# Kernel tuning notes

Hardware: AMD Instinct MI355X
Metric: run time of the kernel (lower is better)

The kernel has to match this reference:

```python
import jax, jax.numpy as jnp
import numpy as np

B, S, D_IN = 2, 2048, 1024
H = 16
HD = 64  # head_dim = d_out // head_cnt


def setup_inputs() -> dict:
    key = jax.random.key(0)
    kx, kq, kk, kv = jax.random.split(key, 4)
    x = jax.random.normal(kx, (B, S, D_IN), dtype=jnp.float32)
    # Per-head Q/K/V projection weights, stacked: [H, d_in, head_dim].
    # Matches nn.Linear(d_in, head_out) per head (qkv_bias=False), scaled like
    # a typical init.
    sc = 1.0 / np.sqrt(D_IN)
    Wq = jax.random.normal(kq, (H, D_IN, HD), dtype=jnp.float32) * sc
    Wk = jax.random.normal(kk, (H, D_IN, HD), dtype=jnp.float32) * sc
    Wv = jax.random.normal(kv, (H, D_IN, HD), dtype=jnp.float32) * sc
    return {"x": x, "Wq": Wq, "Wk": Wk, "Wv": Wv}


def reference(x, Wq, Wk, Wv):
    # Batched multi-head causal attention equivalent to the per-head loop +
    # torch.cat(dim=-1): head h's output occupies slice [h*HD:(h+1)*HD].
    q = jnp.einsum("bsd,hde->bhse", x, Wq)  # [B,H,S,HD]
    k = jnp.einsum("bsd,hde->bhse", x, Wk)
    v = jnp.einsum("bsd,hde->bhse", x, Wv)
    scale = 1.0 / jnp.sqrt(jnp.asarray(HD, dtype=x.dtype))
    scores = jnp.einsum("bhse,bhte->bhst", q, k) * scale  # [B,H,S,S]
    seq = x.shape[1]
    causal = jnp.tril(jnp.ones((seq, seq), dtype=bool))
    scores = jnp.where(causal, scores, jnp.asarray(-jnp.inf, dtype=scores.dtype))
    attn = jax.nn.softmax(scores, axis=-1)  # dropout = 0.0 -> identity
    ctx = jnp.einsum("bhst,bhte->bhse", attn, v)  # [B,H,S,HD]
    # concat heads on last dim
    b, h, s, e = ctx.shape
    return ctx.transpose(0, 2, 1, 3).reshape(b, s, h * e)
```

## Files before the change

kernel.cpp:

```cpp
#include <hip/hip_runtime.h>


#define DI   1024
#define HD   64
#define NH   16
#define SEQ  2048
#define NB   2

typedef unsigned short u16;
typedef unsigned short us8 __attribute__((ext_vector_type(8)));
typedef unsigned short us4 __attribute__((ext_vector_type(4)));
typedef unsigned int   u32x2 __attribute__((ext_vector_type(2)));
typedef short bf8 __attribute__((ext_vector_type(8)));
typedef float f4 __attribute__((ext_vector_type(4)));

#define MFMA16(a, b, c) __builtin_amdgcn_mfma_f32_16x16x32_bf16((a), (b), (c), 0, 0, 0)

#if __has_builtin(__builtin_amdgcn_exp2f)
#define EXP2(x) __builtin_amdgcn_exp2f(x)
#else
#define EXP2(x) exp2f(x)
#endif

#if __has_builtin(__builtin_amdgcn_perm)
#define PKHI(a, b) __builtin_amdgcn_perm((a), (b), 0x07060302u)
#else
__device__ __forceinline__ unsigned PKHI(unsigned a, unsigned b) {
  return (b >> 16) | (a & 0xffff0000u);
}
#endif

__device__ __forceinline__ u16 f2bf(float f) {
  unsigned u = __float_as_uint(f);
  u += 0x7fffu + ((u >> 16) & 1u);
  return (u16)(u >> 16);
}

__device__ __forceinline__ void async16(const u16* g, u16* l) {
  __builtin_amdgcn_global_load_lds((const __attribute__((address_space(1))) void*)g,
                                   (__attribute__((address_space(3))) void*)l,
                                   16, 0, 0);
}

__global__ __launch_bounds__(256) void prep_k(const float* __restrict__ x,
                                              const float* __restrict__ Wq,
                                              const float* __restrict__ Wk,
                                              const float* __restrict__ Wv,
                                              u16* __restrict__ xb,
                                              u16* __restrict__ Wt) {
  __shared__ __align__(16) u16 tile[64][72];
  const int bid = blockIdx.x;
  if (bid < 2048) {
    const int i = (bid * 256 + threadIdx.x) * 8;
    float4 v0 = *(const float4*)(x + i);
    float4 v1 = *(const float4*)(x + i + 4);
    us8 o;
    o[0] = f2bf(v0.x); o[1] = f2bf(v0.y); o[2] = f2bf(v0.z); o[3] = f2bf(v0.w);
    o[4] = f2bf(v1.x); o[5] = f2bf(v1.y); o[6] = f2bf(v1.z); o[7] = f2bf(v1.w);
    *(us8*)(xb + i) = o;
    return;
  }
  const int idx = bid - 2048;
  const int mh = idx >> 4;
  const int d0 = (idx & 15) * 64;
  const int mat = mh >> 4, h = mh & 15;
  const float* W = (mat == 0 ? Wq : (mat == 1 ? Wk : Wv)) + (size_t)h * DI * HD;
  const int t = threadIdx.x;
  {
    const int r = t >> 2, c = (t & 3) * 16;
    const float* src = W + (size_t)(d0 + r) * HD + c;
    #pragma unroll
    for (int j = 0; j < 4; j++) {
      float4 v = *(const float4*)(src + j * 4);
      tile[r][c + j * 4 + 0] = f2bf(v.x);
      tile[r][c + j * 4 + 1] = f2bf(v.y);
      tile[r][c + j * 4 + 2] = f2bf(v.z);
      tile[r][c + j * 4 + 3] = f2bf(v.w);
    }
  }
  __syncthreads();
  {
    const int e = t >> 2, c = (t & 3) * 16;
    __align__(16) u16 tmp[16];
    #pragma unroll
    for (int i = 0; i < 16; i++) tmp[i] = tile[c + i][e];
    u16* dst = Wt + ((size_t)mh * HD + e) * DI + d0 + c;
    *(us8*)dst       = *(us8*)&tmp[0];
    *(us8*)(dst + 8) = *(us8*)&tmp[8];
  }
}

__global__ __launch_bounds__(256) void proj_k(const u16* __restrict__ x,
                                              const u16* __restrict__ Wt,
                                              u16* __restrict__ Qo,
                                              u16* __restrict__ Ko,
                                              u16* __restrict__ Vo) {
  __shared__ __align__(16) u16 xs[128 * 64];
  __shared__ __align__(16) u16 ws[128 * 64];
  const int m0 = blockIdx.x * 128, n0 = blockIdx.y * 128;
  const int tid = threadIdx.x, w = tid >> 6, lane = tid & 63;
  const int l15 = lane & 15, quad = lane >> 4;
  const int lrow = lane >> 3, lch = lane & 7;
  const int l7 = l15 & 7;

  f4 acc[4][4];
  #pragma unroll
  for (int i = 0; i < 4; i++)
    #pragma unroll
    for (int j = 0; j < 4; j++) {
      f4 z = {0.f, 0.f, 0.f, 0.f};
      acc[i][j] = z;
    }

  const u16* xg = x  + (size_t)(m0 + lrow) * DI + ((lch ^ lrow) * 8);
  const u16* wg = Wt + (size_t)(n0 + lrow) * DI + ((lch ^ lrow) * 8);

  for (int k0 = 0; k0 < DI; k0 += 64) {
    #pragma unroll
    for (int i = 0; i < 4; i++) {
      const int r0 = i * 32 + w * 8;
      async16(xg + (size_t)r0 * DI + k0, &xs[r0 * 64]);
      async16(wg + (size_t)r0 * DI + k0, &ws[r0 * 64]);
    }
    __syncthreads();
    #pragma unroll
    for (int ks = 0; ks < 64; ks += 32) {
      const int c0 = (ks >> 3) + quad;
      bf8 af[4], bfr[4];
      #pragma unroll
      for (int i = 0; i < 4; i++)
        af[i] = *(const bf8*)&xs[((w >> 1) * 64 + i * 16 + l15) * 64 + ((c0 ^ l7) * 8)];
      #pragma unroll
      for (int i = 0; i < 4; i++)
        bfr[i] = *(const bf8*)&ws[((w & 1) * 64 + i * 16 + l15) * 64 + ((c0 ^ l7) * 8)];
      #pragma unroll
      for (int mi = 0; mi < 4; mi++)
        #pragma unroll
        for (int ni = 0; ni < 4; ni++)
          acc[mi][ni] = MFMA16(af[mi], bfr[ni], acc[mi][ni]);
    }
    __syncthreads();
  }

  const int mat = n0 >> 10;
  const int nf0 = n0 + (w & 1) * 64;
  const float qscale = 0.125f * 1.44269504088896340736f;
  #pragma unroll
  for (int mi = 0; mi < 4; mi++) {
    const int mrow = m0 + (w >> 1) * 64 + mi * 16 + quad * 4;
    const int b = mrow >> 11, sb = mrow & (SEQ - 1);
    #pragma unroll
    for (int ni = 0; ni < 4; ni++) {
      const int nf = nf0 + ni * 16;
      const int h = (nf >> 6) & 15;
      const int e = (nf & 63) + l15;
      if (mat == 2) {
        __align__(8) u16 pk[4];
        #pragma unroll
        for (int r = 0; r < 4; r++) pk[r] = f2bf(acc[mi][ni][r]);
        *(us4*)(Vo + (((size_t)b * NH + h) * HD + e) * SEQ + sb) = *(us4*)pk;
      } else {
        u16* O = mat ? Ko : Qo;
        const float sc = mat ? 1.0f : qscale;
        #pragma unroll
        for (int r = 0; r < 4; r++)
          O[(((size_t)b * NH + h) * SEQ + sb + r) * HD + e] = f2bf(acc[mi][ni][r] * sc);
      }
    }
  }
}

__global__ __launch_bounds__(256, 2) void attn_k(const u16* __restrict__ Qo,
                                                 const u16* __restrict__ Ko,
                                                 const u16* __restrict__ Vo,
                                                 float* __restrict__ out) {
  __shared__ __align__(16) u16 Ks[2 * 128 * 64];
  __shared__ __align__(16) u16 Vs[2 * 64 * 128];
  __shared__ __align__(16) u16 Ps[4 * 16 * 128];
  const int ia = blockIdx.x;
  const int ib = 31 - ia;
  const int bh = blockIdx.y;
  const int b = bh >> 4, h = bh & 15;
  const int tid = threadIdx.x, w = tid >> 6, lane = tid & 63;
  const int l15 = lane & 15, quad = lane >> 4;
  const int qh = quad >> 1, ql = quad & 1;

  const u16* Qb = Qo + (size_t)bh * SEQ * HD;
  const u16* Kb = Ko + (size_t)bh * SEQ * HD;
  const u16* Vb = Vo + (size_t)bh * HD * SEQ;

  const int qrowA = ia * 64 + w * 16 + l15;
  const int qrowB = ib * 64 + w * 16 + l15;
  bf8 bqA0 = *(const bf8*)(Qb + (size_t)qrowA * HD + quad * 8);
  bf8 bqA1 = *(const bf8*)(Qb + (size_t)qrowA * HD + 32 + quad * 8);
  bf8 bqB0 = *(const bf8*)(Qb + (size_t)qrowB * HD + quad * 8);
  bf8 bqB1 = *(const bf8*)(Qb + (size_t)qrowB * HD + 32 + quad * 8);

  f4 oA[4], oB[4], lA, lB;
  #pragma unroll
  for (int i = 0; i < 4; i++) {
    f4 z = {0.f, 0.f, 0.f, 0.f};
    oA[i] = z; oB[i] = z;
  }
  {
    f4 z = {0.f, 0.f, 0.f, 0.f};
    lA = z; lB = z;
  }
  const bf8 ones = {0x3F80, 0x3F80, 0x3F80, 0x3F80, 0x3F80, 0x3F80, 0x3F80, 0x3F80};

  const int nA = ia / 2 + 1, nB = ib / 2 + 1;

  const u16* ksp0 = &Ks[l15 * 64 + ((quad ^ (l15 & 7)) * 8)];
  const u16* ksp1 = &Ks[l15 * 64 + (((quad + 4) ^ (l15 & 7)) * 8)];
  const u16* vsp[4];
  #pragma unroll
  for (int tc = 0; tc < 4; tc++)
    vsp[tc] = &Vs[l15 * 128 + (((tc * 4 + quad) ^ l15) * 8)];
  u16* const psw = &Ps[w * 2048 + l15 * 128 + ql * 4];
  const u16* prp[4];
  #pragma unroll
  for (int tc = 0; tc < 4; tc++)
    prp[tc] = &Ps[w * 2048 + l15 * 128 + (((tc * 4 + quad) ^ l15) * 8)];

  const int kl = lane >> 3, kc = lane & 7;
  const int vl = lane >> 4, vc = lane & 15;
  const u16* kg = Kb + (size_t)(w * 32 + kl) * HD + ((kc ^ kl) * 8);
  const u16* vg[4];
  u16* ldsK[4];
  u16* ldsV[4];
  #pragma unroll
  for (int i = 0; i < 4; i++) {
    const int vr = w * 16 + i * 4;
    const int f = (i * 4 + vl) & 15;
    vg[i] = Vb + (size_t)(vr + vl) * SEQ + ((vc ^ f) * 8);
    ldsK[i] = &Ks[(w * 32 + i * 8) * 64];
    ldsV[i] = &Vs[vr * 128];
  }

  const int mqA = qrowA - (nA - 1) * 128 - quad * 4;
  const int mqB = qrowB - (nB - 1) * 128 - quad * 4;

  auto pphase = [&](f4* s, bool domask, int mq) {
    #pragma unroll
    for (int mf = 0; mf < 8; mf++) {
      f4 sv = s[mf];
      if (domask) {
        #pragma unroll
        for (int r = 0; r < 4; r++)
          sv[r] = (mf * 16 + r <= mq) ? sv[r] : -1e30f;
      }
      const unsigned p0 = __float_as_uint(EXP2(sv[0]));
      const unsigned p1 = __float_as_uint(EXP2(sv[1]));
      const unsigned p2 = __float_as_uint(EXP2(sv[2]));
      const unsigned p3 = __float_as_uint(EXP2(sv[3]));
      u32x2 pk = {PKHI(p1, p0), PKHI(p3, p2)};
      *(u32x2*)(psw + ((((mf << 1) | qh) ^ l15) * 8)) = pk;
    }
  };

  #pragma unroll
  for (int i = 0; i < 4; i++) {
    async16(kg + i * 512, ldsK[i]);
    async16(vg[i], ldsV[i]);
  }
  kg += 128 * HD;
  #pragma unroll
  for (int i = 0; i < 4; i++) vg[i] += 128;

  for (int it = 0; it < nB; it++) {
    const int cb = (it & 1) * 8192;
    __syncthreads();
    if (it + 1 < nB) {
      const int nb = 8192 - cb;
      #pragma unroll
      for (int i = 0; i < 4; i++) {
        async16(kg + i * 512, ldsK[i] + nb);
        async16(vg[i], ldsV[i] + nb);
      }
      kg += 128 * HD;
      #pragma unroll
      for (int i = 0; i < 4; i++) vg[i] += 128;
    }
    const bool doA = (it < nA);

    f4 sA[8], sB[8];
    #pragma unroll
    for (int mf = 0; mf < 8; mf++) {
      bf8 ak0 = *(const bf8*)(ksp0 + cb + mf * 1024);
      bf8 ak1 = *(const bf8*)(ksp1 + cb + mf * 1024);
      f4 z = {0.f, 0.f, 0.f, 0.f};
      f4 tb = MFMA16(ak0, bqB0, z);
      sB[mf] = MFMA16(ak1, bqB1, tb);
      if (doA) {
        f4 ta = MFMA16(ak0, bqA0, z);
        sA[mf] = MFMA16(ak1, bqA1, ta);
      }
    }

    pphase(sB, it == nB - 1, mqB);
    #pragma unroll
    for (int tc = 0; tc < 4; tc++) {
      bf8 pf = *(const bf8*)(prp[tc]);
      lB = MFMA16(ones, pf, lB);
      #pragma unroll
      for (int ef = 0; ef < 4; ef++) {
        bf8 vf = *(const bf8*)(vsp[tc] + cb + ef * 2048);
        oB[ef] = MFMA16(vf, pf, oB[ef]);
      }
    }
    if (doA) {
      pphase(sA, it == nA - 1, mqA);
      #pragma unroll
      for (int tc = 0; tc < 4; tc++) {
        bf8 pf = *(const bf8*)(prp[tc]);
        lA = MFMA16(ones, pf, lA);
        #pragma unroll
        for (int ef = 0; ef < 4; ef++) {
          bf8 vf = *(const bf8*)(vsp[tc] + cb + ef * 2048);
          oA[ef] = MFMA16(vf, pf, oA[ef]);
        }
      }
    }
  }

  const float invA = 1.0f / lA[0];
  const float invB = 1.0f / lB[0];
  float* opA = out + ((size_t)b * SEQ + qrowA) * (NH * HD) + h * HD + quad * 4;
  float* opB = out + ((size_t)b * SEQ + qrowB) * (NH * HD) + h * HD + quad * 4;
  #pragma unroll
  for (int ef = 0; ef < 4; ef++) {
    f4 va = oA[ef] * invA;
    f4 vb = oB[ef] * invB;
    *(float4*)(opA + ef * 16) = *(float4*)&va;
    *(float4*)(opB + ef * 16) = *(float4*)&vb;
  }
}

extern "C" void kernel_launch(void* const* d_in, const int* in_sizes, int n_in,
                              void* d_out, int out_size, void* d_ws, size_t ws_size,
                              hipStream_t stream) {
  const float* x  = (const float*)d_in[0];
  const float* Wq = (const float*)d_in[1];
  const float* Wk = (const float*)d_in[2];
  const float* Wv = (const float*)d_in[3];
  float* out = (float*)d_out;

  u16* xb = (u16*)d_ws;
  u16* Wt = xb + (size_t)NB * SEQ * DI;
  u16* Qo = Wt + (size_t)3 * NH * HD * DI;
  u16* Ko = Qo + (size_t)NB * NH * SEQ * HD;
  u16* Vo = Ko + (size_t)NB * NH * SEQ * HD;

  prep_k<<<dim3(2048 + 768), 256, 0, stream>>>(x, Wq, Wk, Wv, xb, Wt);
  proj_k<<<dim3(32, 24), 256, 0, stream>>>(xb, Wt, Qo, Ko, Vo);
  attn_k<<<dim3(16, 32), 256, 0, stream>>>(Qo, Ko, Vo, out);
}
```

Before: 158.4 us.

## Double-buffer projection GEMM LDS tiles and widen N tile to 192

The QKV projection GEMM now double-buffers its LDS tiles, issuing the async loads for the next K chunk before computing the current one, and drops one barrier per iteration. The N tile grows from 128 to 192, so each wave computes a 4x6 MFMA block. The grid shrinks to 32x16 and launch bounds request 2 blocks per CU. The goal is to hide global load latency behind MFMA work and raise arithmetic intensity, at the cost of more registers and 80KB of LDS, which may limit occupancy. The head/matrix index is now computed per 16-column fragment, since a 192 tile can straddle Q/K/V boundaries.

```diff
diff --git a/kernel.cpp b/kernel.cpp
--- a/kernel.cpp
+++ b/kernel.cpp
@@ -90,24 +90,25 @@
   }
 }
 
-__global__ __launch_bounds__(256) void proj_k(const u16* __restrict__ x,
-                                              const u16* __restrict__ Wt,
-                                              u16* __restrict__ Qo,
-                                              u16* __restrict__ Ko,
-                                              u16* __restrict__ Vo) {
-  __shared__ __align__(16) u16 xs[128 * 64];
-  __shared__ __align__(16) u16 ws[128 * 64];
-  const int m0 = blockIdx.x * 128, n0 = blockIdx.y * 128;
+__global__ __launch_bounds__(256, 2) void proj_k(const u16* __restrict__ x,
+                                                 const u16* __restrict__ Wt,
+                                                 u16* __restrict__ Qo,
+                                                 u16* __restrict__ Ko,
+                                                 u16* __restrict__ Vo) {
+  __shared__ __align__(16) u16 smem[40960];
+  u16* const xs = smem;
+  u16* const ws = smem + 16384;
+  const int m0 = blockIdx.x * 128, n0 = blockIdx.y * 192;
   const int tid = threadIdx.x, w = tid >> 6, lane = tid & 63;
-  const int l15 = lane & 15, quad = lane >> 4;
+  const int l15 = lane & 15, quad = lane >> 4, l7 = l15 & 7;
   const int lrow = lane >> 3, lch = lane & 7;
-  const int l7 = l15 & 7;
-
-  f4 acc[4][4];
+  const int wm = w >> 1, wn = w & 1;
+
+  f4 acc[4][6];
   #pragma unroll
   for (int i = 0; i < 4; i++)
     #pragma unroll
-    for (int j = 0; j < 4; j++) {
+    for (int j = 0; j < 6; j++) {
       f4 z = {0.f, 0.f, 0.f, 0.f};
       acc[i][j] = z;
     }
@@ -115,43 +116,55 @@
   const u16* xg = x  + (size_t)(m0 + lrow) * DI + ((lch ^ lrow) * 8);
   const u16* wg = Wt + (size_t)(n0 + lrow) * DI + ((lch ^ lrow) * 8);
 
-  for (int k0 = 0; k0 < DI; k0 += 64) {
-    #pragma unroll
-    for (int i = 0; i < 4; i++) {
-      const int r0 = i * 32 + w * 8;
-      async16(xg + (size_t)r0 * DI + k0, &xs[r0 * 64]);
-      async16(wg + (size_t)r0 * DI + k0, &ws[r0 * 64]);
-    }
+  #pragma unroll
+  for (int i = 0; i < 4; i++)
+    async16(xg + (size_t)(i * 32 + w * 8) * DI, &xs[(i * 32 + w * 8) * 64]);
+  #pragma unroll
+  for (int c = 0; c < 6; c++)
+    async16(wg + (size_t)(w * 48 + c * 8) * DI, &ws[(w * 48 + c * 8) * 64]);
+
+  for (int it = 0; it < 16; it++) {
+    const int cbx = (it & 1) * 8192, cbw = (it & 1) * 12288;
     __syncthreads();
+    if (it + 1 < 16) {
+      const int k1 = (it + 1) * 64;
+      const int nbx = 8192 - cbx, nbw = 12288 - cbw;
+      #pragma unroll
+      for (int i = 0; i < 4; i++)
+        async16(xg + (size_t)(i * 32 + w * 8) * DI + k1,
+                &xs[nbx + (i * 32 + w * 8) * 64]);
+      #pragma unroll
+      for (int c = 0; c < 6; c++)
+        async16(wg + (size_t)(w * 48 + c * 8) * DI + k1,
+                &ws[nbw + (w * 48 + c * 8) * 64]);
+    }
     #pragma unroll
     for (int ks = 0; ks < 64; ks += 32) {
       const int c0 = (ks >> 3) + quad;
-      bf8 af[4], bfr[4];
+      bf8 af[4], bfr[6];
       #pragma unroll
       for (int i = 0; i < 4; i++)
-        af[i] = *(const bf8*)&xs[((w >> 1) * 64 + i * 16 + l15) * 64 + ((c0 ^ l7) * 8)];
-      #pragma unroll
-      for (int i = 0; i < 4; i++)
-        bfr[i] = *(const bf8*)&ws[((w & 1) * 64 + i * 16 + l15) * 64 + ((c0 ^ l7) * 8)];
+        af[i] = *(const bf8*)&xs[cbx + (wm * 64 + i * 16 + l15) * 64 + ((c0 ^ l7) * 8)];
+      #pragma unroll
+      for (int i = 0; i < 6; i++)
+        bfr[i] = *(const bf8*)&ws[cbw + (wn * 96 + i * 16 + l15) * 64 + ((c0 ^ l7) * 8)];
       #pragma unroll
       for (int mi = 0; mi < 4; mi++)
         #pragma unroll
-        for (int ni = 0; ni < 4; ni++)
+        for (int ni = 0; ni < 6; ni++)
           acc[mi][ni] = MFMA16(af[mi], bfr[ni], acc[mi][ni]);
     }
-    __syncthreads();
-  }
-
-  const int mat = n0 >> 10;
-  const int nf0 = n0 + (w & 1) * 64;
+  }
+
   const float qscale = 0.125f * 1.44269504088896340736f;
   #pragma unroll
   for (int mi = 0; mi < 4; mi++) {
-    const int mrow = m0 + (w >> 1) * 64 + mi * 16 + quad * 4;
+    const int mrow = m0 + wm * 64 + mi * 16 + quad * 4;
     const int b = mrow >> 11, sb = mrow & (SEQ - 1);
     #pragma unroll
-    for (int ni = 0; ni < 4; ni++) {
-      const int nf = nf0 + ni * 16;
+    for (int ni = 0; ni < 6; ni++) {
+      const int nf = n0 + wn * 96 + ni * 16;
+      const int mat = nf >> 10;
       const int h = (nf >> 6) & 15;
       const int e = (nf & 63) + l15;
       if (mat == 2) {
@@ -352,6 +365,6 @@
   u16* Vo = Ko + (size_t)NB * NH * SEQ * HD;
 
   prep_k<<<dim3(2048 + 768), 256, 0, stream>>>(x, Wq, Wk, Wv, xb, Wt);
-  proj_k<<<dim3(32, 24), 256, 0, stream>>>(xb, Wt, Qo, Ko, Vo);
+  proj_k<<<dim3(32, 16), 256, 0, stream>>>(xb, Wt, Qo, Ko, Vo);
   attn_k<<<dim3(16, 32), 256, 0, stream>>>(Qo, Ko, Vo, out);
 }
```

Result: faster. 143.8 us (-9.2%).
